# Performance work log

Hardware: AMD Instinct MI355X
Metric: run time of the kernel (lower is better)

## Reference

```python
import jax, jax.numpy as jnp
import numpy as np

HEADS = 8
DIM_HEAD = 32
SCALE = DIM_HEAD ** -0.5


def setup_inputs() -> dict:
    key = jax.random.key(0)
    k1, k2, k3 = jax.random.split(key, 3)
    B, L, H, W, C = 2, 5, 100, 176, 256
    inner = HEADS * DIM_HEAD  # 256
    x = jax.random.normal(k1, (B, L, H, W, C), dtype=jnp.float32)
    mask = jnp.ones((B, H, W, 1, L), dtype=jnp.float32)
    W_qkv = jax.random.normal(k2, (C, 3 * inner), dtype=jnp.float32) * (C ** -0.5)
    W_out = jax.random.normal(k3, (inner, C), dtype=jnp.float32) * (inner ** -0.5)
    b_out = jnp.zeros((C,), dtype=jnp.float32)
    return {"x": x, "mask": mask, "W_qkv": W_qkv, "W_out": W_out, "b_out": b_out}


def _cav_attention(x, mask, W_qkv, W_out, b_out):
    B, L, H, W, C = x.shape
    # (B, L, H, W, C) -> (B, H, W, L, C)
    xp = jnp.transpose(x, (0, 2, 3, 1, 4))
    qkv = xp @ W_qkv  # (B,H,W,L,3*inner)
    q, k, v = jnp.split(qkv, 3, axis=-1)

    def to_heads(t):  # (B,H,W,L,m*c) -> (B,m,H,W,L,c)
        t = t.reshape(B, H, W, L, HEADS, DIM_HEAD)
        return jnp.transpose(t, (0, 4, 1, 2, 3, 5))

    q, k, v = to_heads(q), to_heads(k), to_heads(v)
    att = jnp.einsum('bmhwic,bmhwjc->bmhwij', q, k) * SCALE
    # mask: (B,H,W,1,L) -> broadcast over heads as (B,1,H,W,1,L)
    att = jnp.where(mask[:, None] == 0, -jnp.inf, att)
    att = jax.nn.softmax(att, axis=-1)
    out = jnp.einsum('bmhwij,bmhwjc->bmhwic', att, v)
    # (B,m,H,W,L,c) -> (B,H,W,L,m*c)
    out = jnp.transpose(out, (0, 2, 3, 4, 1, 5)).reshape(B, H, W, L, HEADS * DIM_HEAD)
    out = out @ W_out + b_out  # dropout is identity in eval mode
    # (B,H,W,L,C) -> (B,L,H,W,C)
    return jnp.transpose(out, (0, 3, 1, 2, 4))


def reference(x, mask, W_qkv, W_out, b_out):
    return _cav_attention(x, mask, W_qkv, W_out, b_out)
```

## Files before the change

### kernel.cpp

```cpp
#include <hip/hip_runtime.h>
#include <hip/hip_bf16.h>

#define LQ 5
#define HQ 100
#define WQ 176
#define HWQ 17600
#define TPB 8
#define ROWS 40
#define NBLK 4400
#define SCALE_QK 0.17677669529663687f

#define A_OFF 0
#define O_OFF 20480
#define QKV_OFF 40960
#define QBUF_STRIDE 8320
#define GOFS_OFF 74240
#define MASK_OFF 74400
#define SMEM_BYTES 74560

typedef __attribute__((ext_vector_type(8))) short bf16x8;
typedef __attribute__((ext_vector_type(4))) float f32x4;

__device__ __forceinline__ float bf2f(short s) {
  union { unsigned u; float f; } v;
  v.u = ((unsigned)(unsigned short)s) << 16;
  return v.f;
}
__device__ __forceinline__ unsigned short f2bf(float f) {
  union { float f; unsigned u; } v; v.f = f;
  unsigned r = (v.u + 0x7fffu + ((v.u >> 16) & 1u)) >> 16;
  return (unsigned short)r;
}

__global__ void prep_weights(const float* __restrict__ Wqkv,
                             const float* __restrict__ Wout,
                             unsigned short* __restrict__ WqkvT,
                             unsigned short* __restrict__ WoutT) {
  int idx = blockIdx.x * 256 + threadIdx.x;
  if (idx < 256 * 768) {
    int k = idx / 768, n = idx - k * 768;
    WqkvT[n * 256 + k] = f2bf(Wqkv[idx]);
  }
  if (idx < 256 * 256) {
    int k = idx >> 8, n = idx & 255;
    WoutT[n * 256 + k] = f2bf(Wout[idx]);
  }
}

__global__ __launch_bounds__(256, 2)
void cav_attn_fused(const float* __restrict__ x,
                    const float* __restrict__ mask,
                    const unsigned short* __restrict__ WqkvT,
                    const unsigned short* __restrict__ WoutT,
                    const float* __restrict__ b_out,
                    float* __restrict__ out) {
  extern __shared__ char smem[];
  char* A_base = smem + A_OFF;
  char* O_base = smem + O_OFF;
  int*   gofs  = (int*)(smem + GOFS_OFF);
  float* maskv = (float*)(smem + MASK_OFF);

  const int tid  = threadIdx.x;
  const int wave = tid >> 6;
  const int lane = tid & 63;
  const int lr   = lane & 15;
  const int lg   = lane >> 4;
  const int tile0 = blockIdx.x * TPB;

  if (tid < ROWS) {
    int tt = tid / LQ;
    int l  = tid - tt * LQ;
    int gt = tile0 + tt;
    int b  = gt / HWQ;
    int rem = gt - b * HWQ;
    int h  = rem / WQ;
    int w  = rem - h * WQ;
    gofs[tid]  = (((b * LQ + l) * HQ + h) * WQ + w) << 8;
    maskv[tid] = mask[((b * HQ + h) * WQ + w) * LQ + l];
  }
  __syncthreads();

  #pragma unroll
  for (int i = 0; i < 10; ++i) {
    int r  = i * 4 + wave;
    f32x4 v = *(const f32x4*)(x + gofs[r] + lane * 4);
    ushort4 pk;
    pk.x = f2bf(v[0]); pk.y = f2bf(v[1]); pk.z = f2bf(v[2]); pk.w = f2bf(v[3]);
    int byte = r * 512 + lane * 8;
    byte ^= (r & 7) << 4;
    *(ushort4*)(A_base + byte) = pk;
  }
  __syncthreads();

  unsigned short* qbuf = (unsigned short*)(smem + QKV_OFF + wave * QBUF_STRIDE);

  #pragma unroll 1
  for (int hi = 0; hi < 2; ++hi) {
    const int head = wave * 2 + hi;
    f32x4 acc[6][3];
    #pragma unroll
    for (int j = 0; j < 6; ++j)
      #pragma unroll
      for (int mt = 0; mt < 3; ++mt)
        acc[j][mt] = (f32x4){0.f, 0.f, 0.f, 0.f};

    const int hb = head * 32;
    const int nb[6] = { hb, hb + 16, 256 + hb, 256 + hb + 16, 512 + hb, 512 + hb + 16 };

    #pragma unroll
    for (int kt = 0; kt < 8; ++kt) {
      bf16x8 a[3];
      #pragma unroll
      for (int mt = 0; mt < 3; ++mt) {
        int row = mt * 16 + lr;
        int byte = row * 512 + kt * 64 + lg * 16;
        byte ^= (row & 7) << 4;
        a[mt] = *(const bf16x8*)(A_base + byte);
      }
      #pragma unroll
      for (int j = 0; j < 6; ++j) {
        bf16x8 bfr = *(const bf16x8*)(WqkvT + (nb[j] + lr) * 256 + kt * 32 + lg * 8);
        #pragma unroll
        for (int mt = 0; mt < 3; ++mt)
          acc[j][mt] = __builtin_amdgcn_mfma_f32_16x16x32_bf16(a[mt], bfr, acc[j][mt], 0, 0, 0);
      }
    }

    #pragma unroll
    for (int j = 0; j < 6; ++j)
      #pragma unroll
      for (int mt = 0; mt < 3; ++mt)
        #pragma unroll
        for (int rg = 0; rg < 4; ++rg) {
          int row = mt * 16 + lg * 4 + rg;
          if (row < ROWS)
            qbuf[row * 104 + j * 16 + lr] = f2bf(acc[j][mt][rg]);
        }

    if (lane < ROWS) {
      const int t_ = lane / 5;
      const int rq = lane;
      float q[32];
      #pragma unroll
      for (int ch = 0; ch < 4; ++ch) {
        bf16x8 qv = *(const bf16x8*)(qbuf + rq * 104 + ch * 8);
        #pragma unroll
        for (int e = 0; e < 8; ++e) q[ch * 8 + e] = bf2f(qv[e]);
      }
      float p[5];
      #pragma unroll
      for (int j = 0; j < 5; ++j) {
        const int rk = t_ * 5 + j;
        float d = 0.f;
        #pragma unroll
        for (int ch = 0; ch < 4; ++ch) {
          bf16x8 kv = *(const bf16x8*)(qbuf + rk * 104 + 32 + ch * 8);
          #pragma unroll
          for (int e = 0; e < 8; ++e) d += q[ch * 8 + e] * bf2f(kv[e]);
        }
        d *= SCALE_QK;
        p[j] = (maskv[rk] == 0.0f) ? -1e30f : d;
      }
      float mx = fmaxf(fmaxf(fmaxf(p[0], p[1]), fmaxf(p[2], p[3])), p[4]);
      float sum = 0.f;
      #pragma unroll
      for (int j = 0; j < 5; ++j) { p[j] = __expf(p[j] - mx); sum += p[j]; }
      const float inv = 1.0f / sum;
      float o[32];
      #pragma unroll
      for (int c = 0; c < 32; ++c) o[c] = 0.f;
      #pragma unroll
      for (int j = 0; j < 5; ++j) {
        const int rv = t_ * 5 + j;
        const float pj = p[j] * inv;
        #pragma unroll
        for (int ch = 0; ch < 4; ++ch) {
          bf16x8 vv = *(const bf16x8*)(qbuf + rv * 104 + 64 + ch * 8);
          #pragma unroll
          for (int e = 0; e < 8; ++e) o[ch * 8 + e] += pj * bf2f(vv[e]);
        }
      }
      #pragma unroll
      for (int ch = 0; ch < 8; ++ch) {
        ushort4 pk;
        pk.x = f2bf(o[ch * 4 + 0]); pk.y = f2bf(o[ch * 4 + 1]);
        pk.z = f2bf(o[ch * 4 + 2]); pk.w = f2bf(o[ch * 4 + 3]);
        int byte = rq * 512 + head * 64 + ch * 8;
        byte ^= (rq & 7) << 4;
        *(ushort4*)(O_base + byte) = pk;
      }
    }
  }
  __syncthreads();

  f32x4 acc2[4][3];
  #pragma unroll
  for (int j = 0; j < 4; ++j)
    #pragma unroll
    for (int mt = 0; mt < 3; ++mt)
      acc2[j][mt] = (f32x4){0.f, 0.f, 0.f, 0.f};

  #pragma unroll
  for (int kt = 0; kt < 8; ++kt) {
    bf16x8 a[3];
    #pragma unroll
    for (int mt = 0; mt < 3; ++mt) {
      int row = mt * 16 + lr;
      int byte = row * 512 + kt * 64 + lg * 16;
      byte ^= (row & 7) << 4;
      a[mt] = *(const bf16x8*)(O_base + byte);
    }
    #pragma unroll
    for (int j = 0; j < 4; ++j) {
      bf16x8 bfr = *(const bf16x8*)(WoutT + (wave * 64 + j * 16 + lr) * 256 + kt * 32 + lg * 8);
      #pragma unroll
      for (int mt = 0; mt < 3; ++mt)
        acc2[j][mt] = __builtin_amdgcn_mfma_f32_16x16x32_bf16(a[mt], bfr, acc2[j][mt], 0, 0, 0);
    }
  }
  __syncthreads();

  #pragma unroll
  for (int j = 0; j < 4; ++j) {
    const int col = wave * 64 + j * 16 + lr;
    const float bo = b_out[col];
    #pragma unroll
    for (int mt = 0; mt < 3; ++mt)
      #pragma unroll
      for (int rg = 0; rg < 4; ++rg) {
        int row = mt * 16 + lg * 4 + rg;
        if (row < ROWS)
          *(float*)(smem + row * 1024 + col * 4) = acc2[j][mt][rg] + bo;
      }
  }
  __syncthreads();
  #pragma unroll
  for (int i = 0; i < 10; ++i) {
    int r = i * 4 + wave;
    f32x4 v = *(const f32x4*)(smem + r * 1024 + lane * 16);
    *(f32x4*)(out + gofs[r] + lane * 4) = v;
  }
}

extern "C" void kernel_launch(void* const* d_in, const int* in_sizes, int n_in,
                              void* d_out, int out_size, void* d_ws, size_t ws_size,
                              hipStream_t stream) {
  (void)in_sizes; (void)n_in; (void)out_size; (void)ws_size;
  const float* x     = (const float*)d_in[0];
  const float* mask  = (const float*)d_in[1];
  const float* Wqkv  = (const float*)d_in[2];
  const float* Wout  = (const float*)d_in[3];
  const float* bout  = (const float*)d_in[4];
  float* out = (float*)d_out;

  unsigned short* WqkvT = (unsigned short*)d_ws;
  unsigned short* WoutT = WqkvT + 768 * 256;

  (void)hipFuncSetAttribute((const void*)cav_attn_fused,
                            hipFuncAttributeMaxDynamicSharedMemorySize, SMEM_BYTES);

  prep_weights<<<768, 256, 0, stream>>>(Wqkv, Wout, WqkvT, WoutT);
  cav_attn_fused<<<NBLK, 256, SMEM_BYTES, stream>>>(x, mask, WqkvT, WoutT, bout, out);
}
```

Before: 345.2 us.

## Shrink tiles to 30 rows, alias A/O smem, raise occupancy to 4 blocks

Cuts each block from 8 to 6 spatial positions (30 rows, two 16-row MFMA tiles) and reuses the input A buffer for the attention output, roughly halving shared memory so launch bounds can target 4 blocks per CU. The attention step now runs on 60 lanes (two per row, each doing half the head dim) with packed float2 math and a shuffle reduction. Results are held in registers until a barrier and then written into the aliased buffer. The last block is partial and needs bounds handling, and the tighter register budget risks spills.

```diff
diff --git a/kernel.cpp b/kernel.cpp
--- a/kernel.cpp
+++ b/kernel.cpp
@@ -5,32 +5,37 @@
 #define HQ 100
 #define WQ 176
 #define HWQ 17600
-#define TPB 8
-#define ROWS 40
-#define NBLK 4400
+#define NT 35200
+#define TPB 6
+#define ROWS 30
+#define NBLK 5867
 #define SCALE_QK 0.17677669529663687f
 
-#define A_OFF 0
-#define O_OFF 20480
-#define QKV_OFF 40960
-#define QBUF_STRIDE 8320
-#define GOFS_OFF 74240
-#define MASK_OFF 74400
-#define SMEM_BYTES 74560
+#define AO_OFF 0
+#define QBUF_OFF 15360
+#define QBUF_STRIDE 5760
+#define GOFS_OFF 38400
+#define MASK_OFF 38528
+#define SMEM_BYTES 38656
 
 typedef __attribute__((ext_vector_type(8))) short bf16x8;
 typedef __attribute__((ext_vector_type(4))) float f32x4;
-
-__device__ __forceinline__ float bf2f(short s) {
-  union { unsigned u; float f; } v;
-  v.u = ((unsigned)(unsigned short)s) << 16;
-  return v.f;
-}
+typedef __attribute__((ext_vector_type(2))) float f32x2;
+
 __device__ __forceinline__ unsigned short f2bf(float f) {
-  union { float f; unsigned u; } v; v.f = f;
-  unsigned r = (v.u + 0x7fffu + ((v.u >> 16) & 1u)) >> 16;
-  return (unsigned short)r;
-}
+  __hip_bfloat16 b = __float2bfloat16(f);
+  return *(unsigned short*)&b;
+}
+__device__ __forceinline__ f32x2 bfpair(unsigned w) {
+  union { unsigned u; float f; } lo, hi;
+  lo.u = w << 16; hi.u = w & 0xffff0000u;
+  return (f32x2){lo.f, hi.f};
+}
+__device__ __forceinline__ unsigned pack2(f32x2 v) {
+  return ((unsigned)f2bf(v.y) << 16) | (unsigned)f2bf(v.x);
+}
+__device__ __forceinline__ int swzA(int row, int b) { return (row * 512 + b) ^ ((row & 7) << 4); }
+__device__ __forceinline__ int swzQ(int row, int b) { return (row * 192 + b) ^ ((row & 7) << 4); }
 
 __global__ void prep_weights(const float* __restrict__ Wqkv,
                              const float* __restrict__ Wout,
@@ -47,7 +52,94 @@
   }
 }
 
-__global__ __launch_bounds__(256, 2)
+__device__ __forceinline__ void do_head(int head, char* AO, char* qb,
+                                        const unsigned short* __restrict__ WqkvT,
+                                        const float* maskv,
+                                        int lr, int lg, int lane,
+                                        unsigned* oPk ) {
+  f32x4 acc[6][2];
+  #pragma unroll
+  for (int j = 0; j < 6; ++j) {
+    acc[j][0] = (f32x4){0.f, 0.f, 0.f, 0.f};
+    acc[j][1] = (f32x4){0.f, 0.f, 0.f, 0.f};
+  }
+  const int hb = head * 32;
+  const int nb[6] = { hb, hb + 16, 256 + hb, 256 + hb + 16, 512 + hb, 512 + hb + 16 };
+
+  #pragma unroll
+  for (int kt = 0; kt < 8; ++kt) {
+    bf16x8 a0 = *(const bf16x8*)(AO + swzA(lr,      kt * 64 + lg * 16));
+    bf16x8 a1 = *(const bf16x8*)(AO + swzA(16 + lr, kt * 64 + lg * 16));
+    #pragma unroll
+    for (int j = 0; j < 6; ++j) {
+      bf16x8 b = *(const bf16x8*)(WqkvT + (nb[j] + lr) * 256 + kt * 32 + lg * 8);
+      acc[j][0] = __builtin_amdgcn_mfma_f32_16x16x32_bf16(a0, b, acc[j][0], 0, 0, 0);
+      acc[j][1] = __builtin_amdgcn_mfma_f32_16x16x32_bf16(a1, b, acc[j][1], 0, 0, 0);
+    }
+  }
+
+  #pragma unroll
+  for (int j = 0; j < 6; ++j)
+    #pragma unroll
+    for (int mt = 0; mt < 2; ++mt)
+      #pragma unroll
+      for (int rg = 0; rg < 4; ++rg) {
+        int row = mt * 16 + lg * 4 + rg;
+        if (row < ROWS)
+          *(unsigned short*)(qb + swzQ(row, (j * 16 + lr) * 2)) = f2bf(acc[j][mt][rg]);
+      }
+
+  if (lane < 60) {
+    const int r = lane >> 1, h = lane & 1;
+    const int t5 = (r / 5) * 5;
+    uint4 qa = *(const uint4*)(qb + swzQ(r, h * 32));
+    uint4 qc = *(const uint4*)(qb + swzQ(r, h * 32 + 16));
+    f32x2 q2[8];
+    q2[0] = bfpair(qa.x); q2[1] = bfpair(qa.y); q2[2] = bfpair(qa.z); q2[3] = bfpair(qa.w);
+    q2[4] = bfpair(qc.x); q2[5] = bfpair(qc.y); q2[6] = bfpair(qc.z); q2[7] = bfpair(qc.w);
+
+    float p[5];
+    #pragma unroll
+    for (int j = 0; j < 5; ++j) {
+      const int rk = t5 + j;
+      uint4 ka = *(const uint4*)(qb + swzQ(rk, 64 + h * 32));
+      uint4 kc = *(const uint4*)(qb + swzQ(rk, 64 + h * 32 + 16));
+      f32x2 d2 = (f32x2){0.f, 0.f};
+      d2 += q2[0] * bfpair(ka.x); d2 += q2[1] * bfpair(ka.y);
+      d2 += q2[2] * bfpair(ka.z); d2 += q2[3] * bfpair(ka.w);
+      d2 += q2[4] * bfpair(kc.x); d2 += q2[5] * bfpair(kc.y);
+      d2 += q2[6] * bfpair(kc.z); d2 += q2[7] * bfpair(kc.w);
+      float d = d2.x + d2.y;
+      d += __shfl_xor(d, 1);
+      p[j] = (maskv[rk] == 0.0f) ? -1e30f : d * SCALE_QK;
+    }
+    float mx = fmaxf(fmaxf(fmaxf(p[0], p[1]), fmaxf(p[2], p[3])), p[4]);
+    float sum = 0.f;
+    #pragma unroll
+    for (int j = 0; j < 5; ++j) { p[j] = __expf(p[j] - mx); sum += p[j]; }
+    const float inv = 1.0f / sum;
+
+    f32x2 o2[8];
+    #pragma unroll
+    for (int c = 0; c < 8; ++c) o2[c] = (f32x2){0.f, 0.f};
+    #pragma unroll
+    for (int j = 0; j < 5; ++j) {
+      const int rv = t5 + j;
+      uint4 va = *(const uint4*)(qb + swzQ(rv, 128 + h * 32));
+      uint4 vc = *(const uint4*)(qb + swzQ(rv, 128 + h * 32 + 16));
+      f32x2 pj2 = (f32x2){p[j], p[j]};
+      o2[0] += pj2 * bfpair(va.x); o2[1] += pj2 * bfpair(va.y);
+      o2[2] += pj2 * bfpair(va.z); o2[3] += pj2 * bfpair(va.w);
+      o2[4] += pj2 * bfpair(vc.x); o2[5] += pj2 * bfpair(vc.y);
+      o2[6] += pj2 * bfpair(vc.z); o2[7] += pj2 * bfpair(vc.w);
+    }
+    f32x2 inv2 = (f32x2){inv, inv};
+    #pragma unroll
+    for (int c = 0; c < 8; ++c) oPk[c] = pack2(o2[c] * inv2);
+  }
+}
+
+__global__ __launch_bounds__(256, 4)
 void cav_attn_fused(const float* __restrict__ x,
                     const float* __restrict__ mask,
                     const unsigned short* __restrict__ WqkvT,
@@ -55,8 +147,7 @@
                     const float* __restrict__ b_out,
                     float* __restrict__ out) {
   extern __shared__ char smem[];
-  char* A_base = smem + A_OFF;
-  char* O_base = smem + O_OFF;
+  char*  AO    = smem + AO_OFF;
   int*   gofs  = (int*)(smem + GOFS_OFF);
   float* maskv = (float*)(smem + MASK_OFF);
 
@@ -66,156 +157,71 @@
   const int lr   = lane & 15;
   const int lg   = lane >> 4;
   const int tile0 = blockIdx.x * TPB;
+  const int nvalid = (NT - tile0 >= TPB) ? ROWS : (NT - tile0) * LQ;
 
   if (tid < ROWS) {
     int tt = tid / LQ;
     int l  = tid - tt * LQ;
     int gt = tile0 + tt;
-    int b  = gt / HWQ;
-    int rem = gt - b * HWQ;
-    int h  = rem / WQ;
-    int w  = rem - h * WQ;
-    gofs[tid]  = (((b * LQ + l) * HQ + h) * WQ + w) << 8;
-    maskv[tid] = mask[((b * HQ + h) * WQ + w) * LQ + l];
-  }
-  __syncthreads();
-
-  #pragma unroll
-  for (int i = 0; i < 10; ++i) {
-    int r  = i * 4 + wave;
-    f32x4 v = *(const f32x4*)(x + gofs[r] + lane * 4);
-    ushort4 pk;
-    pk.x = f2bf(v[0]); pk.y = f2bf(v[1]); pk.z = f2bf(v[2]); pk.w = f2bf(v[3]);
-    int byte = r * 512 + lane * 8;
-    byte ^= (r & 7) << 4;
-    *(ushort4*)(A_base + byte) = pk;
-  }
-  __syncthreads();
-
-  unsigned short* qbuf = (unsigned short*)(smem + QKV_OFF + wave * QBUF_STRIDE);
-
-  #pragma unroll 1
-  for (int hi = 0; hi < 2; ++hi) {
-    const int head = wave * 2 + hi;
-    f32x4 acc[6][3];
-    #pragma unroll
-    for (int j = 0; j < 6; ++j)
-      #pragma unroll
-      for (int mt = 0; mt < 3; ++mt)
-        acc[j][mt] = (f32x4){0.f, 0.f, 0.f, 0.f};
-
-    const int hb = head * 32;
-    const int nb[6] = { hb, hb + 16, 256 + hb, 256 + hb + 16, 512 + hb, 512 + hb + 16 };
-
-    #pragma unroll
-    for (int kt = 0; kt < 8; ++kt) {
-      bf16x8 a[3];
-      #pragma unroll
-      for (int mt = 0; mt < 3; ++mt) {
-        int row = mt * 16 + lr;
-        int byte = row * 512 + kt * 64 + lg * 16;
-        byte ^= (row & 7) << 4;
-        a[mt] = *(const bf16x8*)(A_base + byte);
-      }
-      #pragma unroll
-      for (int j = 0; j < 6; ++j) {
-        bf16x8 bfr = *(const bf16x8*)(WqkvT + (nb[j] + lr) * 256 + kt * 32 + lg * 8);
-        #pragma unroll
-        for (int mt = 0; mt < 3; ++mt)
-          acc[j][mt] = __builtin_amdgcn_mfma_f32_16x16x32_bf16(a[mt], bfr, acc[j][mt], 0, 0, 0);
-      }
-    }
-
-    #pragma unroll
-    for (int j = 0; j < 6; ++j)
-      #pragma unroll
-      for (int mt = 0; mt < 3; ++mt)
-        #pragma unroll
-        for (int rg = 0; rg < 4; ++rg) {
-          int row = mt * 16 + lg * 4 + rg;
-          if (row < ROWS)
-            qbuf[row * 104 + j * 16 + lr] = f2bf(acc[j][mt][rg]);
-        }
-
-    if (lane < ROWS) {
-      const int t_ = lane / 5;
-      const int rq = lane;
-      float q[32];
-      #pragma unroll
-      for (int ch = 0; ch < 4; ++ch) {
-        bf16x8 qv = *(const bf16x8*)(qbuf + rq * 104 + ch * 8);
-        #pragma unroll
-        for (int e = 0; e < 8; ++e) q[ch * 8 + e] = bf2f(qv[e]);
-      }
-      float p[5];
-      #pragma unroll
-      for (int j = 0; j < 5; ++j) {
-        const int rk = t_ * 5 + j;
-        float d = 0.f;
-        #pragma unroll
-        for (int ch = 0; ch < 4; ++ch) {
-          bf16x8 kv = *(const bf16x8*)(qbuf + rk * 104 + 32 + ch * 8);
-          #pragma unroll
-          for (int e = 0; e < 8; ++e) d += q[ch * 8 + e] * bf2f(kv[e]);
-        }
-        d *= SCALE_QK;
-        p[j] = (maskv[rk] == 0.0f) ? -1e30f : d;
-      }
-      float mx = fmaxf(fmaxf(fmaxf(p[0], p[1]), fmaxf(p[2], p[3])), p[4]);
-      float sum = 0.f;
-      #pragma unroll
-      for (int j = 0; j < 5; ++j) { p[j] = __expf(p[j] - mx); sum += p[j]; }
-      const float inv = 1.0f / sum;
-      float o[32];
-      #pragma unroll
-      for (int c = 0; c < 32; ++c) o[c] = 0.f;
-      #pragma unroll
-      for (int j = 0; j < 5; ++j) {
-        const int rv = t_ * 5 + j;
-        const float pj = p[j] * inv;
-        #pragma unroll
-        for (int ch = 0; ch < 4; ++ch) {
-          bf16x8 vv = *(const bf16x8*)(qbuf + rv * 104 + 64 + ch * 8);
-          #pragma unroll
-          for (int e = 0; e < 8; ++e) o[ch * 8 + e] += pj * bf2f(vv[e]);
-        }
-      }
-      #pragma unroll
-      for (int ch = 0; ch < 8; ++ch) {
-        ushort4 pk;
-        pk.x = f2bf(o[ch * 4 + 0]); pk.y = f2bf(o[ch * 4 + 1]);
-        pk.z = f2bf(o[ch * 4 + 2]); pk.w = f2bf(o[ch * 4 + 3]);
-        int byte = rq * 512 + head * 64 + ch * 8;
-        byte ^= (rq & 7) << 4;
-        *(ushort4*)(O_base + byte) = pk;
-      }
-    }
-  }
-  __syncthreads();
-
-  f32x4 acc2[4][3];
-  #pragma unroll
-  for (int j = 0; j < 4; ++j)
-    #pragma unroll
-    for (int mt = 0; mt < 3; ++mt)
-      acc2[j][mt] = (f32x4){0.f, 0.f, 0.f, 0.f};
-
+    if (gt < NT) {
+      int b = gt / HWQ;
+      int rem = gt - b * HWQ;
+      int h = rem / WQ;
+      int w = rem - h * WQ;
+      gofs[tid]  = (((b * LQ + l) * HQ + h) * WQ + w) << 8;
+      maskv[tid] = mask[((b * HQ + h) * WQ + w) * LQ + l];
+    } else {
+      gofs[tid] = 0;
+      maskv[tid] = 1.0f;
+    }
+  }
+  __syncthreads();
+
+  #pragma unroll
+  for (int i = 0; i < 8; ++i) {
+    int r = i * 4 + wave;
+    if (r < ROWS) {
+      f32x4 v = *(const f32x4*)(x + gofs[r] + lane * 4);
+      ushort4 pk;
+      pk.x = f2bf(v[0]); pk.y = f2bf(v[1]); pk.z = f2bf(v[2]); pk.w = f2bf(v[3]);
+      *(ushort4*)(AO + swzA(r, lane * 8)) = pk;
+    }
+  }
+  __syncthreads();
+
+  char* qb = smem + QBUF_OFF + wave * QBUF_STRIDE;
+  unsigned oPk0[8], oPk1[8];
+  do_head(wave * 2,     AO, qb, WqkvT, maskv, lr, lg, lane, oPk0);
+  do_head(wave * 2 + 1, AO, qb, WqkvT, maskv, lr, lg, lane, oPk1);
+
+  __syncthreads();
+
+  if (lane < 60) {
+    const int r = lane >> 1, h = lane & 1;
+    int b0 = (wave * 2) * 64 + h * 32;
+    *(uint4*)(AO + swzA(r, b0))      = make_uint4(oPk0[0], oPk0[1], oPk0[2], oPk0[3]);
+    *(uint4*)(AO + swzA(r, b0 + 16)) = make_uint4(oPk0[4], oPk0[5], oPk0[6], oPk0[7]);
+    int b1 = (wave * 2 + 1) * 64 + h * 32;
+    *(uint4*)(AO + swzA(r, b1))      = make_uint4(oPk1[0], oPk1[1], oPk1[2], oPk1[3]);
+    *(uint4*)(AO + swzA(r, b1 + 16)) = make_uint4(oPk1[4], oPk1[5], oPk1[6], oPk1[7]);
+  }
+  __syncthreads();
+
+  f32x4 acc2[4][2];
+  #pragma unroll
+  for (int j = 0; j < 4; ++j) {
+    acc2[j][0] = (f32x4){0.f, 0.f, 0.f, 0.f};
+    acc2[j][1] = (f32x4){0.f, 0.f, 0.f, 0.f};
+  }
   #pragma unroll
   for (int kt = 0; kt < 8; ++kt) {
-    bf16x8 a[3];
-    #pragma unroll
-    for (int mt = 0; mt < 3; ++mt) {
-      int row = mt * 16 + lr;
-      int byte = row * 512 + kt * 64 + lg * 16;
-      byte ^= (row & 7) << 4;
-      a[mt] = *(const bf16x8*)(O_base + byte);
-    }
+    bf16x8 a0 = *(const bf16x8*)(AO + swzA(lr,      kt * 64 + lg * 16));
+    bf16x8 a1 = *(const bf16x8*)(AO + swzA(16 + lr, kt * 64 + lg * 16));
     #pragma unroll
     for (int j = 0; j < 4; ++j) {
-      bf16x8 bfr = *(const bf16x8*)(WoutT + (wave * 64 + j * 16 + lr) * 256 + kt * 32 + lg * 8);
-      #pragma unroll
-      for (int mt = 0; mt < 3; ++mt)
-        acc2[j][mt] = __builtin_amdgcn_mfma_f32_16x16x32_bf16(a[mt], bfr, acc2[j][mt], 0, 0, 0);
+      bf16x8 b = *(const bf16x8*)(WoutT + (wave * 64 + j * 16 + lr) * 256 + kt * 32 + lg * 8);
+      acc2[j][0] = __builtin_amdgcn_mfma_f32_16x16x32_bf16(a0, b, acc2[j][0], 0, 0, 0);
+      acc2[j][1] = __builtin_amdgcn_mfma_f32_16x16x32_bf16(a1, b, acc2[j][1], 0, 0, 0);
     }
   }
   __syncthreads();
@@ -225,7 +231,7 @@
     const int col = wave * 64 + j * 16 + lr;
     const float bo = b_out[col];
     #pragma unroll
-    for (int mt = 0; mt < 3; ++mt)
+    for (int mt = 0; mt < 2; ++mt)
       #pragma unroll
       for (int rg = 0; rg < 4; ++rg) {
         int row = mt * 16 + lg * 4 + rg;
@@ -235,10 +241,12 @@
   }
   __syncthreads();
   #pragma unroll
-  for (int i = 0; i < 10; ++i) {
+  for (int i = 0; i < 8; ++i) {
     int r = i * 4 + wave;
-    f32x4 v = *(const f32x4*)(smem + r * 1024 + lane * 16);
-    *(f32x4*)(out + gofs[r] + lane * 4) = v;
+    if (r < nvalid) {
+      f32x4 v = *(const f32x4*)(smem + r * 1024 + lane * 16);
+      *(f32x4*)(out + gofs[r] + lane * 4) = v;
+    }
   }
 }
 
@@ -246,11 +254,11 @@
                               void* d_out, int out_size, void* d_ws, size_t ws_size,
                               hipStream_t stream) {
   (void)in_sizes; (void)n_in; (void)out_size; (void)ws_size;
-  const float* x     = (const float*)d_in[0];
-  const float* mask  = (const float*)d_in[1];
-  const float* Wqkv  = (const float*)d_in[2];
-  const float* Wout  = (const float*)d_in[3];
-  const float* bout  = (const float*)d_in[4];
+  const float* x    = (const float*)d_in[0];
+  const float* mask = (const float*)d_in[1];
+  const float* Wqkv = (const float*)d_in[2];
+  const float* Wout = (const float*)d_in[3];
+  const float* bout = (const float*)d_in[4];
   float* out = (float*)d_out;
 
   unsigned short* WqkvT = (unsigned short*)d_ws;
```

New measurement: 478.6 us. 38.7% more time.
